# Optimization experiments

Measured on AMD Instinct MI355X. Metric: run time of the kernel, lower is better.

The kernel has to match this reference:

```python
import jax, jax.numpy as jnp
import numpy as np

EPS = 1e-05
FACT = 2.0
REJECT_RATIO = 1.0
B, N1, N2 = 8, 4096, 4096


def setup_inputs() -> dict:
    key = jax.random.key(0)
    k1, k2 = jax.random.split(key)
    pc1 = jax.random.normal(k1, (B, 4, N1), dtype=jnp.float32)
    pc2 = jax.random.normal(k2, (B, 4, N2), dtype=jnp.float32)
    # homogeneous coordinates: last row is 1
    pc1 = pc1.at[:, 3, :].set(1.0)
    pc2 = pc2.at[:, 3, :].set(1.0)
    return {"pc1": pc1, "pc2": pc2}


def _rot_to_quat(R):
    # quaternion [w, x, y, z] from 3x3 rotation matrix (branchless)
    def s(x):
        return jnp.where(x >= 0, 1.0, -1.0)
    qw = 0.5 * jnp.sqrt(jnp.maximum(1.0 + R[0, 0] + R[1, 1] + R[2, 2], 1e-12))
    qx = 0.5 * jnp.sqrt(jnp.maximum(1.0 + R[0, 0] - R[1, 1] - R[2, 2], 1e-12)) * s(R[2, 1] - R[1, 2])
    qy = 0.5 * jnp.sqrt(jnp.maximum(1.0 - R[0, 0] + R[1, 1] - R[2, 2], 1e-12)) * s(R[0, 2] - R[2, 0])
    qz = 0.5 * jnp.sqrt(jnp.maximum(1.0 - R[0, 0] - R[1, 1] + R[2, 2], 1e-12)) * s(R[1, 0] - R[0, 1])
    return jnp.stack([qw, qx, qy, qz])


def _single(pc1, pc2):
    # pc1: [4, N1], pc2: [4, N2]
    p1, p2 = pc1[:3], pc2[:3]
    # squared pairwise distance via matmul-expansion trick: [N1, N2]
    d = (jnp.sum(p1 ** 2, axis=0)[:, None]
         - 2.0 * jnp.einsum('dn,dm->nm', p1, p2)
         + jnp.sum(p2 ** 2, axis=0)[None, :])
    # soft nearest neighbor: softmax over N2 of fact / clamp(d, eps)
    w = jax.nn.softmax(FACT / jnp.maximum(d, EPS), axis=1)  # [N1, N2]
    pc_nearest = jnp.einsum('cm,nm->cn', pc2, w)            # [4, N1]

    # soft outlier rejection (near-hard threshold via steep sigmoid)
    dist = jnp.linalg.norm(pc1 - pc_nearest, axis=0)        # [N1]
    mean_dist = jnp.mean(dist)
    indexor = jax.nn.sigmoid((dist - mean_dist * REJECT_RATIO - EPS) * -1e10)

    # weighted Procrustes (soft_tf); note indexor weights BOTH centred clouds
    wsum = jnp.sum(indexor)
    c2 = jnp.sum(pc_nearest[:3] * indexor, axis=-1) / wsum  # [3]
    c1 = jnp.sum(pc1[:3] * indexor, axis=-1) / wsum         # [3]
    p2c = ((pc_nearest[:3] - c2[:, None]) * indexor).T      # [N1, 3]
    p1c = ((pc1[:3] - c1[:, None]) * indexor).T             # [N1, 3]
    H = p1c.T @ p2c                                         # [3, 3]
    U, S, Vh = jnp.linalg.svd(H, full_matrices=False)
    V = Vh.T
    sign = jnp.where(jnp.linalg.det(U) * jnp.linalg.det(V) < 0, -1.0, 1.0)
    V = V * jnp.array([1.0, 1.0, 1.0]).at[2].set(sign)[None, :]  # flip 3rd column
    R = V @ U.T
    t = c2 - R @ c1
    T = jnp.zeros((4, 4), dtype=pc1.dtype)
    T = T.at[:3, :3].set(R).at[:3, 3].set(t).at[3, 3].set(1.0)
    q = _rot_to_quat(R)
    return T, q, t


def reference(pc1, pc2):
    T, q, t = jax.vmap(_single)(pc1, pc2)
    return T, q, t
```

## Files before the change

### kernel.cpp

```cpp
#include <hip/hip_runtime.h>
#include <math.h>


typedef float v2f __attribute__((ext_vector_type(2)));

constexpr int cB  = 8;
constexpr int cN1 = 4096;
constexpr int cN2 = 4096;
constexpr int cMC = 8;
constexpr int cCHUNK = cN2 / cMC;
constexpr int cNB2 = cN1 / 256;
constexpr float cEPS  = 1e-5f;
constexpr float cKK   = 0.34657359027997264f;
constexpr float cEPSK = cEPS * cKK;
constexpr float cUNSC = -1.4426950408889634f;

constexpr size_t OFF_PARTM = 0x400000;
constexpr size_t OFF_DPART = 0x500000;

__global__ __launch_bounds__(256) void cpnet_partial(
    const float* __restrict__ pc1, const float* __restrict__ pc2,
    float4* __restrict__ partA, float* __restrict__ partM) {
  __shared__ float xs[cCHUNK], ys[cCHUNK], zs[cCHUNK], ws[cCHUNK];
  __shared__ float comb[4][256][5];
  const int tid = threadIdx.x;
  const int lane = tid & 63, g = tid >> 6;
  const int b = blockIdx.z, c = blockIdx.y;
  const int nbase = blockIdx.x * 256;

  const float* p2b = pc2 + (size_t)b * 4 * cN2 + c * cCHUNK;
  for (int i = tid; i < cCHUNK; i += 256) {
    float x = p2b[i], y = p2b[cN2 + i], z = p2b[2 * cN2 + i];
    xs[i] = -2.0f * cKK * x;
    ys[i] = -2.0f * cKK * y;
    zs[i] = -2.0f * cKK * z;
    ws[i] = cKK * (x * x + y * y + z * z);
  }
  __syncthreads();

  const float* p1b = pc1 + (size_t)b * 4 * cN1;
  float x1[4], y1[4], z1[4], n1k[4];
#pragma unroll
  for (int k = 0; k < 4; ++k) {
    int r = nbase + k * 64 + lane;
    x1[k] = p1b[r];
    y1[k] = p1b[cN1 + r];
    z1[k] = p1b[2 * cN1 + r];
    n1k[k] = cKK * (x1[k] * x1[k] + y1[k] * y1[k] + z1[k] * z1[k]);
  }

  const v2f* xs2 = (const v2f*)xs + g * 64;
  const v2f* ys2 = (const v2f*)ys + g * 64;
  const v2f* zs2 = (const v2f*)zs + g * 64;
  const v2f* ws2 = (const v2f*)ws + g * 64;

  v2f dmin2[4];
#pragma unroll
  for (int k = 0; k < 4; ++k) dmin2[k] = (v2f){3.0e38f, 3.0e38f};
#pragma unroll 2
  for (int m = 0; m < 64; ++m) {
    v2f vx = xs2[m], vy = ys2[m], vz = zs2[m], vw = ws2[m];
#pragma unroll
    for (int k = 0; k < 4; ++k) {
      v2f dk = vx * x1[k] + (vy * y1[k] + (vz * z1[k] + (vw + n1k[k])));
      dmin2[k] = __builtin_elementwise_min(dmin2[k], dk);
    }
  }
  float M[4];
#pragma unroll
  for (int k = 0; k < 4; ++k)
    M[k] = __builtin_amdgcn_rcpf(fmaxf(fminf(dmin2[k].x, dmin2[k].y), cEPSK));

  v2f S2[4], Ax2[4], Ay2[4], Az2[4];
#pragma unroll
  for (int k = 0; k < 4; ++k) {
    S2[k] = (v2f){0.f, 0.f}; Ax2[k] = (v2f){0.f, 0.f};
    Ay2[k] = (v2f){0.f, 0.f}; Az2[k] = (v2f){0.f, 0.f};
  }
  const v2f EPS2 = {cEPSK, cEPSK};
#pragma unroll 2
  for (int m = 0; m < 64; ++m) {
    v2f vx = xs2[m], vy = ys2[m], vz = zs2[m], vw = ws2[m];
#pragma unroll
    for (int k = 0; k < 4; ++k) {
      v2f dk = vx * x1[k] + (vy * y1[k] + (vz * z1[k] + (vw + n1k[k])));
      dk = __builtin_elementwise_max(dk, EPS2);
      v2f s2v;
      s2v.x = __builtin_amdgcn_rcpf(dk.x);
      s2v.y = __builtin_amdgcn_rcpf(dk.y);
      v2f e;
      e.x = __builtin_amdgcn_exp2f(s2v.x - M[k]);
      e.y = __builtin_amdgcn_exp2f(s2v.y - M[k]);
      S2[k] += e;
      Ax2[k] += e * vx;
      Ay2[k] += e * vy;
      Az2[k] += e * vz;
    }
  }

#pragma unroll
  for (int k = 0; k < 4; ++k) {
    int r = k * 64 + lane;
    comb[g][r][0] = S2[k].x + S2[k].y;
    comb[g][r][1] = Ax2[k].x + Ax2[k].y;
    comb[g][r][2] = Ay2[k].x + Ay2[k].y;
    comb[g][r][3] = Az2[k].x + Az2[k].y;
    comb[g][r][4] = M[k];
  }
  __syncthreads();

  float m0 = comb[0][tid][4], m1 = comb[1][tid][4],
        m2 = comb[2][tid][4], m3 = comb[3][tid][4];
  float mrow = fmaxf(fmaxf(m0, m1), fmaxf(m2, m3));
  float S = 0.f, Ax = 0.f, Ay = 0.f, Az = 0.f;
#pragma unroll
  for (int gg = 0; gg < 4; ++gg) {
    float w = exp2f(comb[gg][tid][4] - mrow);
    S  += comb[gg][tid][0] * w;
    Ax += comb[gg][tid][1] * w;
    Ay += comb[gg][tid][2] * w;
    Az += comb[gg][tid][3] * w;
  }
  const int idx = (c * cB + b) * cN1 + nbase + tid;
  partA[idx] = make_float4(Ax, Ay, Az, S);
  partM[idx] = mrow;
}

__device__ __forceinline__ void reduce_multi(double* v, int nv, double* lds,
                                             int tid) {
  const int lane = tid & 63, w = tid >> 6;
  for (int i = 0; i < nv; ++i) {
    double x = v[i];
    for (int s = 32; s > 0; s >>= 1) x += __shfl_xor(x, s, 64);
    if (lane == 0) lds[i * 4 + w] = x;
  }
  __syncthreads();
  if (tid < nv)
    lds[tid * 4] = lds[tid * 4] + lds[tid * 4 + 1] + lds[tid * 4 + 2] +
                   lds[tid * 4 + 3];
  __syncthreads();
  for (int i = 0; i < nv; ++i) v[i] = lds[i * 4];
  __syncthreads();
}

__global__ __launch_bounds__(256) void cpnet_combine(
    const float* __restrict__ pc1, float4* partA,
    const float* __restrict__ partM, double* __restrict__ dpart) {
  __shared__ double lds[32 * 4];
  const int tid = threadIdx.x;
  const int bx = blockIdx.x, b = blockIdx.y;
  const int n = bx * 256 + tid;

  float Ms[cMC];
  float g = -3.0e38f;
#pragma unroll
  for (int c = 0; c < cMC; ++c) {
    Ms[c] = partM[(c * cB + b) * cN1 + n];
    g = fmaxf(g, Ms[c]);
  }
  float S = 0.f, nx = 0.f, ny = 0.f, nz = 0.f;
#pragma unroll
  for (int c = 0; c < cMC; ++c) {
    float w = exp2f(Ms[c] - g);
    float4 a = partA[(c * cB + b) * cN1 + n];
    S += a.w * w; nx += a.x * w; ny += a.y * w; nz += a.z * w;
  }
  float inv = cUNSC / S;
  nx *= inv; ny *= inv; nz *= inv;
  const float* p1b = pc1 + (size_t)b * 4 * cN1;
  float dx = p1b[n] - nx, dy = p1b[cN1 + n] - ny, dz = p1b[2 * cN1 + n] - nz;
  float dist = sqrtf(dx * dx + dy * dy + dz * dz);
  partA[(0 * cB + b) * cN1 + n] = make_float4(nx, ny, nz, dist);

  double acc[1];
  acc[0] = (double)dist;
  reduce_multi(acc, 1, lds, tid);
  if (tid == 0) dpart[b * cNB2 + bx] = acc[0];
}

__global__ __launch_bounds__(256) void cpnet_moments_solve(
    const float* __restrict__ pc1, const float4* __restrict__ partA,
    const double* __restrict__ dpart, float* __restrict__ out) {
  __shared__ double lds[23 * 4];
  const int tid = threadIdx.x;
  const int b = blockIdx.x;
  const float* p1b = pc1 + (size_t)b * 4 * cN1;

  double dsum = 0.0;
  for (int i = 0; i < cNB2; ++i) dsum += dpart[b * cNB2 + i];
  const float meanf = (float)(dsum * (1.0 / (double)cN1));

  double a[23];
  for (int i = 0; i < 23; ++i) a[i] = 0.0;
  for (int it = 0; it < cNB2; ++it) {
    const int n = it * 256 + tid;
    float4 nn = partA[(0 * cB + b) * cN1 + n];
    float u = (nn.w - meanf - cEPS) * 1e10f;
    float ind = 1.0f / (1.0f + expf(u));
    double di = (double)ind, di2 = di * di;
    double x1 = (double)p1b[n], y1 = (double)p1b[cN1 + n],
           z1 = (double)p1b[2 * cN1 + n];
    double x2 = (double)nn.x, y2 = (double)nn.y, z2 = (double)nn.z;

    a[0] += di;
    a[1] += di * x1;  a[2] += di * y1;  a[3] += di * z1;
    a[4] += di * x2;  a[5] += di * y2;  a[6] += di * z2;
    a[7] += di2;
    a[8]  += di2 * x1;  a[9]  += di2 * y1;  a[10] += di2 * z1;
    a[11] += di2 * x2;  a[12] += di2 * y2;  a[13] += di2 * z2;
    a[14] += di2 * x1 * x2; a[15] += di2 * x1 * y2; a[16] += di2 * x1 * z2;
    a[17] += di2 * y1 * x2; a[18] += di2 * y1 * y2; a[19] += di2 * y1 * z2;
    a[20] += di2 * z1 * x2; a[21] += di2 * z1 * y2; a[22] += di2 * z1 * z2;
  }
  reduce_multi(a, 23, lds, tid);

  if (tid != 0) return;

  double W = a[0];
  double c1[3] = {a[1] / W, a[2] / W, a[3] / W};
  double c2[3] = {a[4] / W, a[5] / W, a[6] / W};
  double H[3][3];
  for (int i = 0; i < 3; ++i)
    for (int j = 0; j < 3; ++j)
      H[i][j] = a[14 + 3 * i + j] - c2[j] * a[8 + i] -
                c1[i] * a[11 + j] + c1[i] * c2[j] * a[7];

  double trH = H[0][0] + H[1][1] + H[2][2];
  double Nm[4][4], V[4][4];
  Nm[0][0] = trH;
  Nm[0][1] = Nm[1][0] = H[1][2] - H[2][1];
  Nm[0][2] = Nm[2][0] = H[2][0] - H[0][2];
  Nm[0][3] = Nm[3][0] = H[0][1] - H[1][0];
  Nm[1][1] = 2.0 * H[0][0] - trH;
  Nm[1][2] = Nm[2][1] = H[0][1] + H[1][0];
  Nm[1][3] = Nm[3][1] = H[0][2] + H[2][0];
  Nm[2][2] = 2.0 * H[1][1] - trH;
  Nm[2][3] = Nm[3][2] = H[1][2] + H[2][1];
  Nm[3][3] = 2.0 * H[2][2] - trH;

  for (int i = 0; i < 4; ++i)
    for (int j = 0; j < 4; ++j) V[i][j] = (i == j) ? 1.0 : 0.0;

  for (int sweep = 0; sweep < 6; ++sweep) {
    for (int p = 0; p < 3; ++p) {
      for (int q = p + 1; q < 4; ++q) {
        double apq = Nm[p][q];
        if (fabs(apq) < 1e-300) continue;
        double theta = (Nm[q][q] - Nm[p][p]) / (2.0 * apq);
        double tt = (theta >= 0.0 ? 1.0 : -1.0) /
                    (fabs(theta) + sqrt(theta * theta + 1.0));
        double cc = 1.0 / sqrt(tt * tt + 1.0);
        double ss = tt * cc;
        for (int k = 0; k < 4; ++k) {
          double akp = Nm[k][p], akq = Nm[k][q];
          Nm[k][p] = cc * akp - ss * akq;
          Nm[k][q] = ss * akp + cc * akq;
        }
        for (int k = 0; k < 4; ++k) {
          double apk = Nm[p][k], aqk = Nm[q][k];
          Nm[p][k] = cc * apk - ss * aqk;
          Nm[q][k] = ss * apk + cc * aqk;
        }
        for (int k = 0; k < 4; ++k) {
          double vkp = V[k][p], vkq = V[k][q];
          V[k][p] = cc * vkp - ss * vkq;
          V[k][q] = ss * vkp + cc * vkq;
        }
      }
    }
  }
  int imax = 0;
  for (int i = 1; i < 4; ++i)
    if (Nm[i][i] > Nm[imax][imax]) imax = i;
  double qw = V[0][imax], qx = V[1][imax], qy = V[2][imax], qz = V[3][imax];
  double qn = sqrt(qw * qw + qx * qx + qy * qy + qz * qz);
  qw /= qn; qx /= qn; qy /= qn; qz /= qn;

  double R[3][3];
  R[0][0] = 1.0 - 2.0 * (qy * qy + qz * qz);
  R[0][1] = 2.0 * (qx * qy - qw * qz);
  R[0][2] = 2.0 * (qx * qz + qw * qy);
  R[1][0] = 2.0 * (qx * qy + qw * qz);
  R[1][1] = 1.0 - 2.0 * (qx * qx + qz * qz);
  R[1][2] = 2.0 * (qy * qz - qw * qx);
  R[2][0] = 2.0 * (qx * qz - qw * qy);
  R[2][1] = 2.0 * (qy * qz + qw * qx);
  R[2][2] = 1.0 - 2.0 * (qx * qx + qy * qy);

  double tr1 = 0.0, tr2 = 0.0;
  for (int i = 0; i < 3; ++i)
    for (int j = 0; j < 3; ++j) {
      tr1 += R[i][j] * H[j][i];
      tr2 += R[j][i] * H[j][i];
    }
  if (tr2 > tr1) {
    for (int i = 0; i < 3; ++i)
      for (int j = i + 1; j < 3; ++j) {
        double tmp = R[i][j]; R[i][j] = R[j][i]; R[j][i] = tmp;
      }
  }

  double tx = c2[0] - (R[0][0] * c1[0] + R[0][1] * c1[1] + R[0][2] * c1[2]);
  double ty = c2[1] - (R[1][0] * c1[0] + R[1][1] * c1[1] + R[1][2] * c1[2]);
  double tz = c2[2] - (R[2][0] * c1[0] + R[2][1] * c1[1] + R[2][2] * c1[2]);

  auto sgn = [](double x) { return x >= 0.0 ? 1.0 : -1.0; };
  double oqw = 0.5 * sqrt(fmax(1.0 + R[0][0] + R[1][1] + R[2][2], 1e-12));
  double oqx = 0.5 * sqrt(fmax(1.0 + R[0][0] - R[1][1] - R[2][2], 1e-12)) *
               sgn(R[2][1] - R[1][2]);
  double oqy = 0.5 * sqrt(fmax(1.0 - R[0][0] + R[1][1] - R[2][2], 1e-12)) *
               sgn(R[0][2] - R[2][0]);
  double oqz = 0.5 * sqrt(fmax(1.0 - R[0][0] - R[1][1] + R[2][2], 1e-12)) *
               sgn(R[1][0] - R[0][1]);

  float* T = out + b * 16;
  T[0]  = (float)R[0][0]; T[1]  = (float)R[0][1]; T[2]  = (float)R[0][2]; T[3]  = (float)tx;
  T[4]  = (float)R[1][0]; T[5]  = (float)R[1][1]; T[6]  = (float)R[1][2]; T[7]  = (float)ty;
  T[8]  = (float)R[2][0]; T[9]  = (float)R[2][1]; T[10] = (float)R[2][2]; T[11] = (float)tz;
  T[12] = 0.f; T[13] = 0.f; T[14] = 0.f; T[15] = 1.f;
  float* Q = out + 128 + b * 4;
  Q[0] = (float)oqw; Q[1] = (float)oqx; Q[2] = (float)oqy; Q[3] = (float)oqz;
  float* Tt = out + 160 + b * 3;
  Tt[0] = (float)tx; Tt[1] = (float)ty; Tt[2] = (float)tz;
}

extern "C" void kernel_launch(void* const* d_in, const int* in_sizes, int n_in,
                              void* d_out, int out_size, void* d_ws, size_t ws_size,
                              hipStream_t stream) {
  const float* pc1 = (const float*)d_in[0];
  const float* pc2 = (const float*)d_in[1];
  float* out = (float*)d_out;
  char* ws = (char*)d_ws;

  float4* partA = (float4*)ws;
  float*  partM = (float*)(ws + OFF_PARTM);
  double* dpart = (double*)(ws + OFF_DPART);

  cpnet_partial<<<dim3(cN1 / 256, cMC, cB), 256, 0, stream>>>(pc1, pc2,
                                                              partA, partM);
  cpnet_combine<<<dim3(cNB2, cB), 256, 0, stream>>>(pc1, partA, partM, dpart);
  cpnet_moments_solve<<<cB, 256, 0, stream>>>(pc1, partA, dpart, out);
}
```

Baseline: 138.0 us.

## Compute pairwise distances with split-bf16 MFMA instead of scalar FMA loops

Replaces the per-thread FMA distance computation with 16x16x32 bf16 MFMA, encoding each coordinate as hi+lo bf16 pairs to approximate fp32 accuracy. The point data is reorganised into MFMA fragment layouts in shared memory, and per-row min and softmax sums are reduced with cross-lane shuffles instead of an LDS combine step. This offloads the distance arithmetic to matrix cores, but the exp/rcp transcendental work per pair is unchanged and is probably the real bottleneck. It also adds shuffle reductions and risks precision loss from the bf16 split, which matters because 2/d is amplified near small distances.

```diff
diff --git a/kernel.cpp b/kernel.cpp
--- a/kernel.cpp
+++ b/kernel.cpp
@@ -2,7 +2,9 @@
 #include <math.h>
 
 
-typedef float v2f __attribute__((ext_vector_type(2)));
+typedef float f32x4 __attribute__((ext_vector_type(4)));
+typedef short s16x8 __attribute__((ext_vector_type(8)));
+typedef unsigned short u16;
 
 constexpr int cB  = 8;
 constexpr int cN1 = 4096;
@@ -18,112 +20,157 @@
 constexpr size_t OFF_PARTM = 0x400000;
 constexpr size_t OFF_DPART = 0x500000;
 
+__device__ __forceinline__ u16 f2bf(float f) {
+  unsigned u = __builtin_bit_cast(unsigned, f);
+  u += 0x7FFFu + ((u >> 16) & 1u);
+  return (u16)(u >> 16);
+}
+__device__ __forceinline__ float bfhi(float f) {
+  unsigned u = __builtin_bit_cast(unsigned, f);
+  u += 0x7FFFu + ((u >> 16) & 1u);
+  u &= 0xFFFF0000u;
+  return __builtin_bit_cast(float, u);
+}
+__device__ __forceinline__ f32x4 shfl_xor4(f32x4 v, int m) {
+  f32x4 o;
+  o.x = __shfl_xor(v.x, m, 64);
+  o.y = __shfl_xor(v.y, m, 64);
+  o.z = __shfl_xor(v.z, m, 64);
+  o.w = __shfl_xor(v.w, m, 64);
+  return o;
+}
+
 __global__ __launch_bounds__(256) void cpnet_partial(
     const float* __restrict__ pc1, const float* __restrict__ pc2,
     float4* __restrict__ partA, float* __restrict__ partM) {
-  __shared__ float xs[cCHUNK], ys[cCHUNK], zs[cCHUNK], ws[cCHUNK];
-  __shared__ float comb[4][256][5];
+  __shared__ s16x8 bfrag[32][2][16];
+  __shared__ float4 vxyz[cCHUNK];
   const int tid = threadIdx.x;
-  const int lane = tid & 63, g = tid >> 6;
-  const int b = blockIdx.z, c = blockIdx.y;
+  const int lane = tid & 63, wv = tid >> 6;
+  const int g = lane >> 4, c = lane & 15;
+  const int b = blockIdx.z, ch = blockIdx.y;
   const int nbase = blockIdx.x * 256;
 
-  const float* p2b = pc2 + (size_t)b * 4 * cN2 + c * cCHUNK;
-  for (int i = tid; i < cCHUNK; i += 256) {
-    float x = p2b[i], y = p2b[cN2 + i], z = p2b[2 * cN2 + i];
-    xs[i] = -2.0f * cKK * x;
-    ys[i] = -2.0f * cKK * y;
-    zs[i] = -2.0f * cKK * z;
-    ws[i] = cKK * (x * x + y * y + z * z);
+  const float* p2b = pc2 + (size_t)b * 4 * cN2 + ch * cCHUNK;
+  for (int e = tid; e < 1024; e += 256) {
+    int t = e >> 5, gg = (e >> 4) & 1, cc = e & 15;
+    int m = t * 16 + cc;
+    float x = p2b[m], y = p2b[cN2 + m], z = p2b[2 * cN2 + m];
+    float X = -2.0f * cKK * x, Y = -2.0f * cKK * y, Z = -2.0f * cKK * z;
+    float w = cKK * (x * x + y * y + z * z);
+    u16 xh = f2bf(X), yh = f2bf(Y), zh = f2bf(Z), wh = f2bf(w);
+    u16 xl = f2bf(X - bfhi(X)), yl = f2bf(Y - bfhi(Y));
+    u16 zl = f2bf(Z - bfhi(Z)), wl = f2bf(w - bfhi(w));
+    s16x8 fr;
+    if (gg == 0) {
+      fr = (s16x8){(short)xh, (short)yh, (short)zh, (short)xh,
+                   (short)yh, (short)zh, (short)xl, (short)yl};
+      vxyz[m] = make_float4(X, Y, Z, 0.f);
+    } else {
+      fr = (s16x8){(short)zl, (short)xl, (short)yl, (short)zl,
+                   (short)0x3F80, (short)0x3F80, (short)wh, (short)wl};
+    }
+    bfrag[t][gg][cc] = fr;
   }
   __syncthreads();
 
   const float* p1b = pc1 + (size_t)b * 4 * cN1;
-  float x1[4], y1[4], z1[4], n1k[4];
-#pragma unroll
-  for (int k = 0; k < 4; ++k) {
-    int r = nbase + k * 64 + lane;
-    x1[k] = p1b[r];
-    y1[k] = p1b[cN1 + r];
-    z1[k] = p1b[2 * cN1 + r];
-    n1k[k] = cKK * (x1[k] * x1[k] + y1[k] * y1[k] + z1[k] * z1[k]);
-  }
-
-  const v2f* xs2 = (const v2f*)xs + g * 64;
-  const v2f* ys2 = (const v2f*)ys + g * 64;
-  const v2f* zs2 = (const v2f*)zs + g * 64;
-  const v2f* ws2 = (const v2f*)ws + g * 64;
-
-  v2f dmin2[4];
-#pragma unroll
-  for (int k = 0; k < 4; ++k) dmin2[k] = (v2f){3.0e38f, 3.0e38f};
-#pragma unroll 2
-  for (int m = 0; m < 64; ++m) {
-    v2f vx = xs2[m], vy = ys2[m], vz = zs2[m], vw = ws2[m];
-#pragma unroll
-    for (int k = 0; k < 4; ++k) {
-      v2f dk = vx * x1[k] + (vy * y1[k] + (vz * z1[k] + (vw + n1k[k])));
-      dmin2[k] = __builtin_elementwise_min(dmin2[k], dk);
-    }
-  }
-  float M[4];
-#pragma unroll
-  for (int k = 0; k < 4; ++k)
-    M[k] = __builtin_amdgcn_rcpf(fmaxf(fminf(dmin2[k].x, dmin2[k].y), cEPSK));
-
-  v2f S2[4], Ax2[4], Ay2[4], Az2[4];
-#pragma unroll
-  for (int k = 0; k < 4; ++k) {
-    S2[k] = (v2f){0.f, 0.f}; Ax2[k] = (v2f){0.f, 0.f};
-    Ay2[k] = (v2f){0.f, 0.f}; Az2[k] = (v2f){0.f, 0.f};
-  }
-  const v2f EPS2 = {cEPSK, cEPSK};
-#pragma unroll 2
-  for (int m = 0; m < 64; ++m) {
-    v2f vx = xs2[m], vy = ys2[m], vz = zs2[m], vw = ws2[m];
-#pragma unroll
-    for (int k = 0; k < 4; ++k) {
-      v2f dk = vx * x1[k] + (vy * y1[k] + (vz * z1[k] + (vw + n1k[k])));
-      dk = __builtin_elementwise_max(dk, EPS2);
-      v2f s2v;
-      s2v.x = __builtin_amdgcn_rcpf(dk.x);
-      s2v.y = __builtin_amdgcn_rcpf(dk.y);
-      v2f e;
-      e.x = __builtin_amdgcn_exp2f(s2v.x - M[k]);
-      e.y = __builtin_amdgcn_exp2f(s2v.y - M[k]);
-      S2[k] += e;
-      Ax2[k] += e * vx;
-      Ay2[k] += e * vy;
-      Az2[k] += e * vz;
-    }
-  }
-
-#pragma unroll
-  for (int k = 0; k < 4; ++k) {
-    int r = k * 64 + lane;
-    comb[g][r][0] = S2[k].x + S2[k].y;
-    comb[g][r][1] = Ax2[k].x + Ax2[k].y;
-    comb[g][r][2] = Ay2[k].x + Ay2[k].y;
-    comb[g][r][3] = Az2[k].x + Az2[k].y;
-    comb[g][r][4] = M[k];
-  }
-  __syncthreads();
-
-  float m0 = comb[0][tid][4], m1 = comb[1][tid][4],
-        m2 = comb[2][tid][4], m3 = comb[3][tid][4];
-  float mrow = fmaxf(fmaxf(m0, m1), fmaxf(m2, m3));
-  float S = 0.f, Ax = 0.f, Ay = 0.f, Az = 0.f;
-#pragma unroll
-  for (int gg = 0; gg < 4; ++gg) {
-    float w = exp2f(comb[gg][tid][4] - mrow);
-    S  += comb[gg][tid][0] * w;
-    Ax += comb[gg][tid][1] * w;
-    Ay += comb[gg][tid][2] * w;
-    Az += comb[gg][tid][3] * w;
-  }
-  const int idx = (c * cB + b) * cN1 + nbase + tid;
-  partA[idx] = make_float4(Ax, Ay, Az, S);
-  partM[idx] = mrow;
+  s16x8 afr[4];
+  if (g < 2) {
+#pragma unroll
+    for (int rt = 0; rt < 4; ++rt) {
+      int r = nbase + wv * 64 + rt * 16 + c;
+      float x = p1b[r], y = p1b[cN1 + r], z = p1b[2 * cN1 + r];
+      float nk = cKK * (x * x + y * y + z * z);
+      u16 xh = f2bf(x), yh = f2bf(y), zh = f2bf(z), nh = f2bf(nk);
+      u16 xl = f2bf(x - bfhi(x)), yl = f2bf(y - bfhi(y));
+      u16 zl = f2bf(z - bfhi(z)), nl = f2bf(nk - bfhi(nk));
+      afr[rt] = (g == 0)
+          ? (s16x8){(short)xh, (short)yh, (short)zh, (short)xl,
+                    (short)yl, (short)zl, (short)xh, (short)yh}
+          : (s16x8){(short)zh, (short)xl, (short)yl, (short)zl,
+                    (short)nh, (short)nl, (short)0x3F80, (short)0x3F80};
+    }
+  } else {
+#pragma unroll
+    for (int rt = 0; rt < 4; ++rt) afr[rt] = (s16x8){0, 0, 0, 0, 0, 0, 0, 0};
+  }
+  const s16x8 bzero = (s16x8){0, 0, 0, 0, 0, 0, 0, 0};
+  const f32x4 czero = (f32x4){0.f, 0.f, 0.f, 0.f};
+
+  f32x4 dmin[4];
+#pragma unroll
+  for (int rt = 0; rt < 4; ++rt)
+    dmin[rt] = (f32x4){3.0e38f, 3.0e38f, 3.0e38f, 3.0e38f};
+  for (int t = 0; t < 32; ++t) {
+    s16x8 bf = (g < 2) ? bfrag[t][g][c] : bzero;
+#pragma unroll
+    for (int rt = 0; rt < 4; ++rt) {
+      f32x4 D = __builtin_amdgcn_mfma_f32_16x16x32_bf16(afr[rt], bf, czero,
+                                                        0, 0, 0);
+      dmin[rt] = __builtin_elementwise_min(dmin[rt], D);
+    }
+  }
+  f32x4 Mv[4];
+#pragma unroll
+  for (int rt = 0; rt < 4; ++rt) {
+#pragma unroll
+    for (int s = 1; s < 16; s <<= 1)
+      dmin[rt] = __builtin_elementwise_min(dmin[rt], shfl_xor4(dmin[rt], s));
+    f32x4 Mrt;
+    Mrt.x = __builtin_amdgcn_rcpf(fmaxf(dmin[rt].x, cEPSK));
+    Mrt.y = __builtin_amdgcn_rcpf(fmaxf(dmin[rt].y, cEPSK));
+    Mrt.z = __builtin_amdgcn_rcpf(fmaxf(dmin[rt].z, cEPSK));
+    Mrt.w = __builtin_amdgcn_rcpf(fmaxf(dmin[rt].w, cEPSK));
+    Mv[rt] = Mrt;
+  }
+
+  f32x4 accS[4], accX[4], accY[4], accZ[4];
+#pragma unroll
+  for (int rt = 0; rt < 4; ++rt) {
+    accS[rt] = czero; accX[rt] = czero; accY[rt] = czero; accZ[rt] = czero;
+  }
+  const f32x4 EPS4 = (f32x4){cEPSK, cEPSK, cEPSK, cEPSK};
+  for (int t = 0; t < 32; ++t) {
+    s16x8 bf = (g < 2) ? bfrag[t][g][c] : bzero;
+    float4 v = vxyz[t * 16 + c];
+#pragma unroll
+    for (int rt = 0; rt < 4; ++rt) {
+      f32x4 D = __builtin_amdgcn_mfma_f32_16x16x32_bf16(afr[rt], bf, czero,
+                                                        0, 0, 0);
+      f32x4 dk = __builtin_elementwise_max(D, EPS4);
+      f32x4 e;
+      e.x = __builtin_amdgcn_exp2f(__builtin_amdgcn_rcpf(dk.x) - Mv[rt].x);
+      e.y = __builtin_amdgcn_exp2f(__builtin_amdgcn_rcpf(dk.y) - Mv[rt].y);
+      e.z = __builtin_amdgcn_exp2f(__builtin_amdgcn_rcpf(dk.z) - Mv[rt].z);
+      e.w = __builtin_amdgcn_exp2f(__builtin_amdgcn_rcpf(dk.w) - Mv[rt].w);
+      accS[rt] += e;
+      accX[rt] += e * v.x;
+      accY[rt] += e * v.y;
+      accZ[rt] += e * v.z;
+    }
+  }
+
+  const int idxb = (ch * cB + b) * cN1;
+#pragma unroll
+  for (int rt = 0; rt < 4; ++rt) {
+#pragma unroll
+    for (int s = 1; s < 16; s <<= 1) {
+      accS[rt] += shfl_xor4(accS[rt], s);
+      accX[rt] += shfl_xor4(accX[rt], s);
+      accY[rt] += shfl_xor4(accY[rt], s);
+      accZ[rt] += shfl_xor4(accZ[rt], s);
+    }
+    if (c == 0) {
+      int rowbase = nbase + wv * 64 + rt * 16 + g * 4;
+#pragma unroll
+      for (int r = 0; r < 4; ++r) {
+        partA[idxb + rowbase + r] =
+            make_float4(accX[rt][r], accY[rt][r], accZ[rt][r], accS[rt][r]);
+        partM[idxb + rowbase + r] = Mv[rt][r];
+      }
+    }
+  }
 }
 
 __device__ __forceinline__ void reduce_multi(double* v, int nv, double* lds,
```

Measured after the change: 182.9 us. 1.33x slower.
